# Optimization experiments

Hardware: AMD Instinct MI355X
Metric: run time of the kernel (lower is better)

Reference implementation:

```python
import jax, jax.numpy as jnp
import numpy as np

N_HEADS = 8
TANH_CLIP = 10.0
NEG = -1e9  # finite stand-in for -inf so log_softmax/vjp stay NaN-free


def setup_inputs() -> dict:
    key = jax.random.key(0)
    ks = jax.random.split(key, 8)
    B, N, D = 256, 1000, 128
    embeddings = jax.random.normal(ks[0], (B, N, D), dtype=jnp.float32)
    W_node = jax.random.normal(ks[1], (D, 3 * D), dtype=jnp.float32) * (1.0 / np.sqrt(D))
    W_fixed = jax.random.normal(ks[2], (D, D), dtype=jnp.float32) * (1.0 / np.sqrt(D))
    W_step = jax.random.normal(ks[3], (2 * D, D), dtype=jnp.float32) * (1.0 / np.sqrt(2 * D))
    W_out = jax.random.normal(ks[4], (D, D), dtype=jnp.float32) * (1.0 / np.sqrt(D))
    first_idx = jax.random.randint(ks[5], (B,), 0, N)
    last_idx = jax.random.randint(ks[6], (B,), 0, N)
    mask = jax.random.randint(ks[7], (B, N), 0, 2).astype(jnp.bool_)
    mask = mask.at[:, 0].set(False)  # guarantee at least one feasible node
    return {"embeddings": embeddings, "W_node": W_node, "W_fixed": W_fixed,
            "W_step": W_step, "W_out": W_out, "first_idx": first_idx,
            "last_idx": last_idx, "mask": mask}


def reference(embeddings, W_node, W_fixed, W_step, W_out, first_idx, last_idx, mask):
    # One pointer-network decode step (TSP variant of AttentionModel._get_log_p),
    # including the _precompute projections.
    B, N, D = embeddings.shape
    H = N_HEADS
    dk = D // H

    # _precompute: fixed context + glimpse K/V + logit key
    graph_embed = embeddings.mean(axis=1)                       # [B, D]
    fixed_ctx = graph_embed @ W_fixed                           # [B, D]
    kvl = embeddings @ W_node                                   # [B, N, 3D]
    K, V, logit_K = jnp.split(kvl, 3, axis=-1)                  # each [B, N, D]

    # step context: cat(first-node emb, last-node emb) -> project to D
    b = jnp.arange(B)
    step_ctx = jnp.concatenate([embeddings[b, first_idx], embeddings[b, last_idx]], axis=-1)  # [B, 2D]
    q = fixed_ctx + step_ctx @ W_step                           # [B, D]

    # masked multi-head glimpse attention (q_len = 1)
    qh = q.reshape(B, H, dk)                                    # [B, H, dk]
    Kh = K.reshape(B, N, H, dk)
    Vh = V.reshape(B, N, H, dk)
    compat = jnp.einsum('bhd,bnhd->bhn', qh, Kh) / np.sqrt(dk)  # [B, H, N]
    compat = jnp.where(mask[:, None, :], NEG, compat)           # mask_inner
    attn = jax.nn.softmax(compat, axis=-1)
    heads = jnp.einsum('bhn,bnhd->bhd', attn, Vh)               # [B, H, dk]
    glimpse = heads.reshape(B, D) @ W_out                       # [B, D]

    # single-head logit attention with tanh clipping
    logits = jnp.einsum('bd,bnd->bn', glimpse, logit_K) / np.sqrt(D)  # [B, N]
    logits = jnp.tanh(logits) * TANH_CLIP
    logits = jnp.where(mask, NEG, logits)                       # mask_logits
    return jax.nn.log_softmax(logits, axis=-1)                  # [B, N]
```

## Files before the change

### kernel.cpp

```cpp
#include <hip/hip_runtime.h>


#define NEG (-1e9f)

__global__ __launch_bounds__(1024) void k_fused(
    const float* __restrict__ E, const float* __restrict__ Wn,
    const float* __restrict__ Wf, const float* __restrict__ Ws,
    const float* __restrict__ Wo,
    const int* __restrict__ fi, const int* __restrict__ li,
    const int* __restrict__ maskI, const unsigned char* __restrict__ maskB,
    float* __restrict__ out)
{
    const int b = blockIdx.x;
    const int t = threadIdx.x;

    __shared__ float4 Et[4096];
    __shared__ float4 qk4[256];
    __shared__ float4 pt4[256];
    __shared__ float4 EbarF4[256];
    __shared__ float4 mu4[32], e14[32], e24[32], gp4[32];
    __shared__ float q[128], heads[128], gl[128];
    __shared__ float qred[8][128];
    __shared__ float ct[128 * 9];
    __shared__ float redh[72];
    __shared__ float mh[8], lh[8], al[8];
    __shared__ float red[16];
    __shared__ float stat[2];
    __shared__ int flagS;

    float* const mu = (float*)mu4;
    float* const e1 = (float*)e14;
    float* const e2 = (float*)e24;
    float* const gp = (float*)gp4;
    float* const pt = (float*)pt4;
    float* const EbarF = (float*)EbarF4;
    float* const qkf = (float*)qk4;

    const float4* E4 = (const float4*)(E + (size_t)b * 128000);

    if (t == 0) flagS = 0;
    const uint4 dv = ((const uint4*)maskI)[t];
    const unsigned det = (dv.x | dv.y | dv.z | dv.w) & 0xFFFFFF00u;

    {
        const int cm = t & 31, sm = t >> 5;
        float4 acc = make_float4(0.f, 0.f, 0.f, 0.f);
        for (int r = sm; r < 1000; r += 32) {
            const float4 v = E4[r * 32 + cm];
            acc.x += v.x; acc.y += v.y; acc.z += v.z; acc.w += v.w;
        }
        Et[t] = acc;
    }
    if (t >= 512 && t < 544) {
        e14[t - 512] = E4[fi[b] * 32 + (t - 512)];
    } else if (t >= 544 && t < 576) {
        e24[t - 544] = E4[li[b] * 32 + (t - 544)];
    }
    __syncthreads();
    if (det) atomicOr(&flagS, 1);
    if (t < 32) {
        float4 acc = Et[t];
        #pragma unroll
        for (int s = 1; s < 32; ++s) {
            const float4 v = Et[s * 32 + t];
            acc.x += v.x; acc.y += v.y; acc.z += v.z; acc.w += v.w;
        }
        const float inv = 1.0f / 1000.0f;
        mu4[t] = make_float4(acc.x * inv, acc.y * inv, acc.z * inv, acc.w * inv);
    }
    __syncthreads();

    {
        const int part = t >> 7, d = t & 127;
        float acc = 0.f;
        const int k0 = part * 48;
        for (int k = k0; k < k0 + 48; ++k) {
            const float s = (k < 128) ? mu[k] : (k < 256 ? e1[k - 128] : e2[k - 256]);
            const float w = (k < 128) ? Wf[k * 128 + d] : Ws[(k - 128) * 128 + d];
            acc += s * w;
        }
        qred[part][d] = acc;
    }
    __syncthreads();
    if (t < 128) {
        float acc = 0.f;
        #pragma unroll
        for (int p = 0; p < 8; ++p) acc += qred[p][t];
        q[t] = acc;
    }
    __syncthreads();
    {
        const int j = t & 127, cg = t >> 7;
        const float qj = q[j];
        for (int c0 = 0; c0 < 128; c0 += 8) {
            const int c = c0 + cg;
            float v = Wn[c * 384 + j] * qj;
            v += __shfl_down(v, 8, 16);
            v += __shfl_down(v, 4, 16);
            v += __shfl_down(v, 2, 16);
            v += __shfl_down(v, 1, 16);
            if ((j & 15) == 0) {
                const int h = j >> 4, s = c >> 2;
                qkf[h * 128 + (s ^ (s >> 2)) * 4 + (c & 3)] = v * 0.25f;
            }
        }
    }
    __syncthreads();

    const bool useB = (flagS != 0);

    if (t < 8) { mh[t] = -3e38f; lh[t] = 0.f; }
    float4 eacc[8];
    #pragma unroll
    for (int h = 0; h < 8; ++h) eacc[h] = make_float4(0.f, 0.f, 0.f, 0.f);
    const int c4 = t & 31, sl = t >> 5;
    const int rr = t >> 3, qq = t & 7;

    for (int tile = 0; tile < 8; ++tile) {
        const int r0 = tile * 128;
        {
            const int g = r0 + rr;
            float4 v[4];
            if (g < 1000) {
                #pragma unroll
                for (int i = 0; i < 4; ++i) v[i] = E4[g * 32 + qq * 4 + i];
            } else {
                #pragma unroll
                for (int i = 0; i < 4; ++i) v[i] = make_float4(0.f, 0.f, 0.f, 0.f);
            }
            float pch[8];
            #pragma unroll
            for (int h = 0; h < 8; ++h) pch[h] = 0.f;
            #pragma unroll
            for (int i = 0; i < 4; ++i) {
                const int grp = qq * 4 + i;
                Et[rr * 32 + (grp ^ (rr & 7))] = v[i];
                const int sg = grp ^ (grp >> 2);
                #pragma unroll
                for (int h = 0; h < 8; ++h) {
                    const float4 w = qk4[h * 32 + sg];
                    pch[h] += v[i].x * w.x + v[i].y * w.y + v[i].z * w.z + v[i].w * w.w;
                }
            }
            #pragma unroll
            for (int m = 1; m <= 4; m <<= 1) {
                #pragma unroll
                for (int h = 0; h < 8; ++h) pch[h] += __shfl_xor(pch[h], m, 64);
            }
            bool msk = (g >= 1000);
            if (!msk) msk = useB ? (maskB[b * 1000 + g] != 0)
                                 : (maskI[b * 1000 + g] != 0);
            ct[rr * 9 + qq] = msk ? NEG : pch[qq];
        }
        __syncthreads();
        if (t < 64) {
            const int h = t & 7, part = t >> 3;
            float mt = -3e38f;
            const int rb = part * 16;
            for (int r = 0; r < 16; ++r) mt = fmaxf(mt, ct[(rb + r) * 9 + h]);
            redh[part * 9 + h] = mt;
        }
        __syncthreads();
        if (t < 8) {
            float mt = redh[t];
            for (int p = 1; p < 8; ++p) mt = fmaxf(mt, redh[p * 9 + t]);
            const float mnew = fmaxf(mh[t], mt);
            al[t] = __expf(mh[t] - mnew);
            mh[t] = mnew;
        }
        __syncthreads();
        {
            const int row = t >> 3, h = t & 7;
            pt[row * 8 + h] = __expf(ct[row * 9 + h] - mh[h]);
        }
        __syncthreads();
        {
            #pragma unroll
            for (int h = 0; h < 8; ++h) {
                const float a = al[h];
                eacc[h].x *= a; eacc[h].y *= a; eacc[h].z *= a; eacc[h].w *= a;
            }
            #pragma unroll
            for (int j = 0; j < 4; ++j) {
                const int r = sl * 4 + j;
                const float4 ev = Et[r * 32 + (c4 ^ (r & 7))];
                const float4 p0 = pt4[r * 2];
                const float4 p1 = pt4[r * 2 + 1];
                eacc[0].x += p0.x * ev.x; eacc[0].y += p0.x * ev.y; eacc[0].z += p0.x * ev.z; eacc[0].w += p0.x * ev.w;
                eacc[1].x += p0.y * ev.x; eacc[1].y += p0.y * ev.y; eacc[1].z += p0.y * ev.z; eacc[1].w += p0.y * ev.w;
                eacc[2].x += p0.z * ev.x; eacc[2].y += p0.z * ev.y; eacc[2].z += p0.z * ev.z; eacc[2].w += p0.z * ev.w;
                eacc[3].x += p0.w * ev.x; eacc[3].y += p0.w * ev.y; eacc[3].z += p0.w * ev.z; eacc[3].w += p0.w * ev.w;
                eacc[4].x += p1.x * ev.x; eacc[4].y += p1.x * ev.y; eacc[4].z += p1.x * ev.z; eacc[4].w += p1.x * ev.w;
                eacc[5].x += p1.y * ev.x; eacc[5].y += p1.y * ev.y; eacc[5].z += p1.y * ev.z; eacc[5].w += p1.y * ev.w;
                eacc[6].x += p1.z * ev.x; eacc[6].y += p1.z * ev.y; eacc[6].z += p1.z * ev.z; eacc[6].w += p1.z * ev.w;
                eacc[7].x += p1.w * ev.x; eacc[7].y += p1.w * ev.y; eacc[7].z += p1.w * ev.z; eacc[7].w += p1.w * ev.w;
            }
        }
        if (t < 64) {
            const int h = t & 7, part = t >> 3;
            float s = 0.f;
            const int rb = part * 16;
            for (int r = 0; r < 16; ++r) s += pt[(rb + r) * 8 + h];
            redh[part * 9 + h] = s;
        }
        __syncthreads();
        if (t < 8) {
            float s = 0.f;
            for (int p = 0; p < 8; ++p) s += redh[p * 9 + t];
            lh[t] = lh[t] * al[t] + s;
        }
    }

    if (sl >= 16) {
        #pragma unroll
        for (int h = 0; h < 8; ++h) Et[(sl - 16) * 256 + h * 32 + c4] = eacc[h];
    }
    __syncthreads();
    if (sl < 16) {
        #pragma unroll
        for (int h = 0; h < 8; ++h) {
            const float4 o = Et[sl * 256 + h * 32 + c4];
            eacc[h].x += o.x; eacc[h].y += o.y; eacc[h].z += o.z; eacc[h].w += o.w;
            Et[sl * 256 + h * 32 + c4] = eacc[h];
        }
    }
    __syncthreads();
    if (t < 256) {
        const int h = t >> 5, cc = t & 31;
        float4 s = make_float4(0.f, 0.f, 0.f, 0.f);
        #pragma unroll
        for (int s2 = 0; s2 < 16; ++s2) {
            const float4 v = Et[s2 * 256 + h * 32 + cc];
            s.x += v.x; s.y += v.y; s.z += v.z; s.w += v.w;
        }
        const float invl = 1.0f / lh[h];
        EbarF4[h * 32 + cc] = make_float4(s.x * invl, s.y * invl, s.z * invl, s.w * invl);
    }
    __syncthreads();

    {
        const int part = t >> 7, d = t & 127, h = d >> 4;
        float acc = 0.f;
        const int c0 = part * 16;
        for (int c = c0; c < c0 + 16; ++c) acc += EbarF[h * 128 + c] * Wn[c * 384 + 128 + d];
        qred[part][d] = acc;
    }
    __syncthreads();
    if (t < 128) {
        float acc = 0.f;
        #pragma unroll
        for (int p = 0; p < 8; ++p) acc += qred[p][t];
        heads[t] = acc;
    }
    __syncthreads();
    {
        const int part = t >> 7, d = t & 127;
        float acc = 0.f;
        const int j0 = part * 16;
        for (int j = j0; j < j0 + 16; ++j) acc += heads[j] * Wo[j * 128 + d];
        qred[part][d] = acc;
    }
    __syncthreads();
    if (t < 128) {
        float acc = 0.f;
        #pragma unroll
        for (int p = 0; p < 8; ++p) acc += qred[p][t];
        gl[t] = acc;
    }
    __syncthreads();
    {
        const int part = t >> 7, c = t & 127;
        float acc = 0.f;
        const int d0 = part * 16;
        for (int d = d0; d < d0 + 16; ++d) acc += Wn[c * 384 + 256 + d] * gl[d];
        qred[part][c] = acc;
    }
    __syncthreads();
    if (t < 128) {
        float acc = 0.f;
        #pragma unroll
        for (int p = 0; p < 8; ++p) acc += qred[p][t];
        gp[t] = acc * 0.08838834764831845f;
    }
    __syncthreads();

    {
        const int row = t >> 3, sub = t & 7;
        for (int tile = 0; tile < 8; ++tile) {
            const int g = tile * 128 + row;
            float acc = 0.f;
            if (g < 1000) {
                #pragma unroll
                for (int i = 0; i < 4; ++i) {
                    const float4 v = E4[g * 32 + sub * 4 + i];
                    const float4 w = gp4[sub * 4 + i];
                    acc += v.x * w.x + v.y * w.y + v.z * w.z + v.w * w.w;
                }
            }
            ct[row * 9 + sub] = acc;
            __syncthreads();
            if (t < 128) {
                const int g2 = tile * 128 + t;
                if (g2 < 1000) {
                    float s = 0.f;
                    #pragma unroll
                    for (int k = 0; k < 8; ++k) s += ct[t * 9 + k];
                    float zz = 10.0f * tanhf(s);
                    const bool m = useB ? (maskB[b * 1000 + g2] != 0)
                                        : (maskI[b * 1000 + g2] != 0);
                    if (m) zz = NEG;
                    pt[g2] = zz;
                }
            }
            __syncthreads();
        }
    }
    float v = (t < 1000) ? pt[t] : -3e38f;
    #pragma unroll
    for (int off = 32; off > 0; off >>= 1) v = fmaxf(v, __shfl_down(v, off, 64));
    if ((t & 63) == 0) red[t >> 6] = v;
    __syncthreads();
    if (t == 0) {
        float m = red[0];
        for (int i = 1; i < 16; ++i) m = fmaxf(m, red[i]);
        stat[0] = m;
    }
    __syncthreads();
    float sv = (t < 1000) ? __expf(pt[t] - stat[0]) : 0.f;
    #pragma unroll
    for (int off = 32; off > 0; off >>= 1) sv += __shfl_down(sv, off, 64);
    if ((t & 63) == 0) red[t >> 6] = sv;
    __syncthreads();
    if (t == 0) {
        float s = 0.f;
        for (int i = 0; i < 16; ++i) s += red[i];
        stat[1] = stat[0] + __logf(s);
    }
    __syncthreads();
    if (t < 1000)
        out[(size_t)b * 1000 + t] = pt[t] - stat[1];
}

extern "C" void kernel_launch(void* const* d_in, const int* in_sizes, int n_in,
                              void* d_out, int out_size, void* d_ws, size_t ws_size,
                              hipStream_t stream) {
    const float* E  = (const float*)d_in[0];
    const float* Wn = (const float*)d_in[1];
    const float* Wf = (const float*)d_in[2];
    const float* Ws = (const float*)d_in[3];
    const float* Wo = (const float*)d_in[4];
    const int*   fi = (const int*)d_in[5];
    const int*   li = (const int*)d_in[6];
    const int*   maskI = (const int*)d_in[7];
    const unsigned char* maskB = (const unsigned char*)d_in[7];
    float* out = (float*)d_out;

    k_fused<<<256, 1024, 0, stream>>>(E, Wn, Wf, Ws, Wo, fi, li, maskI, maskB, out);
}
```

Measured before the change: 281.8 us.

## Prefetch next embedding tile, fuse softmax reductions, and drop barriers in decode loop

Register-prefetches the next 128-row embedding tile while the current tile is processed, and loads the first tile before the mean-pooling pass. The per-tile max and sum reductions now use wave shuffles instead of two-stage shared-memory reductions. Exponentials are recomputed inline in the weighted-sum loop rather than staged through shared memory, which removes several barriers per tile. The logit pass also reduces with shuffles and no per-tile barriers. In exchange it raises register pressure at 1024 threads and duplicates the exp work.

```diff
diff --git a/kernel.cpp b/kernel.cpp
--- a/kernel.cpp
+++ b/kernel.cpp
@@ -22,7 +22,6 @@
     __shared__ float q[128], heads[128], gl[128];
     __shared__ float qred[8][128];
     __shared__ float ct[128 * 9];
-    __shared__ float redh[72];
     __shared__ float mh[8], lh[8], al[8];
     __shared__ float red[16];
     __shared__ float stat[2];
@@ -41,6 +40,13 @@
     if (t == 0) flagS = 0;
     const uint4 dv = ((const uint4*)maskI)[t];
     const unsigned det = (dv.x | dv.y | dv.z | dv.w) & 0xFFFFFF00u;
+
+    const int rr = t >> 3, qq = t & 7;
+    const int c4 = t & 31, sl = t >> 5;
+
+    float4 vcur[4];
+    #pragma unroll
+    for (int i = 0; i < 4; ++i) vcur[i] = E4[rr * 32 + qq * 4 + i];
 
     {
         const int cm = t & 31, sm = t >> 5;
@@ -105,41 +111,41 @@
             }
         }
     }
+    if (t < 8) { mh[t] = -3e38f; lh[t] = 0.f; }
     __syncthreads();
 
     const bool useB = (flagS != 0);
 
-    if (t < 8) { mh[t] = -3e38f; lh[t] = 0.f; }
     float4 eacc[8];
     #pragma unroll
     for (int h = 0; h < 8; ++h) eacc[h] = make_float4(0.f, 0.f, 0.f, 0.f);
-    const int c4 = t & 31, sl = t >> 5;
-    const int rr = t >> 3, qq = t & 7;
 
     for (int tile = 0; tile < 8; ++tile) {
-        const int r0 = tile * 128;
+        float4 vnext[4];
+        if (tile < 7) {
+            const int gn = (tile + 1) * 128 + rr;
+            if (gn < 1000) {
+                #pragma unroll
+                for (int i = 0; i < 4; ++i) vnext[i] = E4[gn * 32 + qq * 4 + i];
+            } else {
+                #pragma unroll
+                for (int i = 0; i < 4; ++i) vnext[i] = make_float4(0.f, 0.f, 0.f, 0.f);
+            }
+        }
         {
-            const int g = r0 + rr;
-            float4 v[4];
-            if (g < 1000) {
-                #pragma unroll
-                for (int i = 0; i < 4; ++i) v[i] = E4[g * 32 + qq * 4 + i];
-            } else {
-                #pragma unroll
-                for (int i = 0; i < 4; ++i) v[i] = make_float4(0.f, 0.f, 0.f, 0.f);
-            }
+            const int g = tile * 128 + rr;
             float pch[8];
             #pragma unroll
             for (int h = 0; h < 8; ++h) pch[h] = 0.f;
             #pragma unroll
             for (int i = 0; i < 4; ++i) {
                 const int grp = qq * 4 + i;
-                Et[rr * 32 + (grp ^ (rr & 7))] = v[i];
+                Et[rr * 32 + (grp ^ (rr & 7))] = vcur[i];
                 const int sg = grp ^ (grp >> 2);
                 #pragma unroll
                 for (int h = 0; h < 8; ++h) {
                     const float4 w = qk4[h * 32 + sg];
-                    pch[h] += v[i].x * w.x + v[i].y * w.y + v[i].z * w.z + v[i].w * w.w;
+                    pch[h] += vcur[i].x * w.x + vcur[i].y * w.y + vcur[i].z * w.z + vcur[i].w * w.w;
                 }
             }
             #pragma unroll
@@ -154,61 +160,57 @@
         }
         __syncthreads();
         if (t < 64) {
-            const int h = t & 7, part = t >> 3;
+            const int h = t >> 3, j = t & 7;
             float mt = -3e38f;
-            const int rb = part * 16;
-            for (int r = 0; r < 16; ++r) mt = fmaxf(mt, ct[(rb + r) * 9 + h]);
-            redh[part * 9 + h] = mt;
-        }
-        __syncthreads();
-        if (t < 8) {
-            float mt = redh[t];
-            for (int p = 1; p < 8; ++p) mt = fmaxf(mt, redh[p * 9 + t]);
-            const float mnew = fmaxf(mh[t], mt);
-            al[t] = __expf(mh[t] - mnew);
-            mh[t] = mnew;
+            for (int r = j; r < 128; r += 8) mt = fmaxf(mt, ct[r * 9 + h]);
+            mt = fmaxf(mt, __shfl_xor(mt, 1, 64));
+            mt = fmaxf(mt, __shfl_xor(mt, 2, 64));
+            mt = fmaxf(mt, __shfl_xor(mt, 4, 64));
+            if (j == 0) {
+                const float mnew = fmaxf(mh[h], mt);
+                al[h] = __expf(mh[h] - mnew);
+                mh[h] = mnew;
+            }
         }
         __syncthreads();
         {
-            const int row = t >> 3, h = t & 7;
-            pt[row * 8 + h] = __expf(ct[row * 9 + h] - mh[h]);
+            float alr[8], mhr[8];
+            #pragma unroll
+            for (int h = 0; h < 8; ++h) { alr[h] = al[h]; mhr[h] = mh[h]; }
+            #pragma unroll
+            for (int h = 0; h < 8; ++h) {
+                eacc[h].x *= alr[h]; eacc[h].y *= alr[h];
+                eacc[h].z *= alr[h]; eacc[h].w *= alr[h];
+            }
+            #pragma unroll
+            for (int j2 = 0; j2 < 4; ++j2) {
+                const int r = sl * 4 + j2;
+                const float4 ev = Et[r * 32 + (c4 ^ (r & 7))];
+                float p[8];
+                #pragma unroll
+                for (int h = 0; h < 8; ++h) p[h] = __expf(ct[r * 9 + h] - mhr[h]);
+                #pragma unroll
+                for (int h = 0; h < 8; ++h) {
+                    eacc[h].x += p[h] * ev.x; eacc[h].y += p[h] * ev.y;
+                    eacc[h].z += p[h] * ev.z; eacc[h].w += p[h] * ev.w;
+                }
+            }
+        }
+        if (t < 64) {
+            const int h = t >> 3, j = t & 7;
+            const float mhh = mh[h];
+            float s = 0.f;
+            for (int r = j; r < 128; r += 8) s += __expf(ct[r * 9 + h] - mhh);
+            s += __shfl_xor(s, 1, 64);
+            s += __shfl_xor(s, 2, 64);
+            s += __shfl_xor(s, 4, 64);
+            if (j == 0) lh[h] = lh[h] * al[h] + s;
+        }
+        if (tile < 7) {
+            #pragma unroll
+            for (int i = 0; i < 4; ++i) vcur[i] = vnext[i];
         }
         __syncthreads();
-        {
-            #pragma unroll
-            for (int h = 0; h < 8; ++h) {
-                const float a = al[h];
-                eacc[h].x *= a; eacc[h].y *= a; eacc[h].z *= a; eacc[h].w *= a;
-            }
-            #pragma unroll
-            for (int j = 0; j < 4; ++j) {
-                const int r = sl * 4 + j;
-                const float4 ev = Et[r * 32 + (c4 ^ (r & 7))];
-                const float4 p0 = pt4[r * 2];
-                const float4 p1 = pt4[r * 2 + 1];
-                eacc[0].x += p0.x * ev.x; eacc[0].y += p0.x * ev.y; eacc[0].z += p0.x * ev.z; eacc[0].w += p0.x * ev.w;
-                eacc[1].x += p0.y * ev.x; eacc[1].y += p0.y * ev.y; eacc[1].z += p0.y * ev.z; eacc[1].w += p0.y * ev.w;
-                eacc[2].x += p0.z * ev.x; eacc[2].y += p0.z * ev.y; eacc[2].z += p0.z * ev.z; eacc[2].w += p0.z * ev.w;
-                eacc[3].x += p0.w * ev.x; eacc[3].y += p0.w * ev.y; eacc[3].z += p0.w * ev.z; eacc[3].w += p0.w * ev.w;
-                eacc[4].x += p1.x * ev.x; eacc[4].y += p1.x * ev.y; eacc[4].z += p1.x * ev.z; eacc[4].w += p1.x * ev.w;
-                eacc[5].x += p1.y * ev.x; eacc[5].y += p1.y * ev.y; eacc[5].z += p1.y * ev.z; eacc[5].w += p1.y * ev.w;
-                eacc[6].x += p1.z * ev.x; eacc[6].y += p1.z * ev.y; eacc[6].z += p1.z * ev.z; eacc[6].w += p1.z * ev.w;
-                eacc[7].x += p1.w * ev.x; eacc[7].y += p1.w * ev.y; eacc[7].z += p1.w * ev.z; eacc[7].w += p1.w * ev.w;
-            }
-        }
-        if (t < 64) {
-            const int h = t & 7, part = t >> 3;
-            float s = 0.f;
-            const int rb = part * 16;
-            for (int r = 0; r < 16; ++r) s += pt[(rb + r) * 8 + h];
-            redh[part * 9 + h] = s;
-        }
-        __syncthreads();
-        if (t < 8) {
-            float s = 0.f;
-            for (int p = 0; p < 8; ++p) s += redh[p * 9 + t];
-            lh[t] = lh[t] * al[t] + s;
-        }
     }
 
     if (sl >= 16) {
@@ -284,37 +286,29 @@
     }
     __syncthreads();
 
-    {
-        const int row = t >> 3, sub = t & 7;
-        for (int tile = 0; tile < 8; ++tile) {
-            const int g = tile * 128 + row;
-            float acc = 0.f;
-            if (g < 1000) {
-                #pragma unroll
-                for (int i = 0; i < 4; ++i) {
-                    const float4 v = E4[g * 32 + sub * 4 + i];
-                    const float4 w = gp4[sub * 4 + i];
-                    acc += v.x * w.x + v.y * w.y + v.z * w.z + v.w * w.w;
-                }
-            }
-            ct[row * 9 + sub] = acc;
-            __syncthreads();
-            if (t < 128) {
-                const int g2 = tile * 128 + t;
-                if (g2 < 1000) {
-                    float s = 0.f;
-                    #pragma unroll
-                    for (int k = 0; k < 8; ++k) s += ct[t * 9 + k];
-                    float zz = 10.0f * tanhf(s);
-                    const bool m = useB ? (maskB[b * 1000 + g2] != 0)
-                                        : (maskI[b * 1000 + g2] != 0);
-                    if (m) zz = NEG;
-                    pt[g2] = zz;
-                }
-            }
-            __syncthreads();
-        }
-    }
+    for (int tile = 0; tile < 8; ++tile) {
+        const int g = tile * 128 + rr;
+        float acc = 0.f;
+        if (g < 1000) {
+            #pragma unroll
+            for (int i = 0; i < 4; ++i) {
+                const float4 v = E4[g * 32 + qq * 4 + i];
+                const float4 w = gp4[qq * 4 + i];
+                acc += v.x * w.x + v.y * w.y + v.z * w.z + v.w * w.w;
+            }
+        }
+        acc += __shfl_xor(acc, 1, 64);
+        acc += __shfl_xor(acc, 2, 64);
+        acc += __shfl_xor(acc, 4, 64);
+        if (qq == 0 && g < 1000) {
+            float zz = 10.0f * tanhf(acc);
+            const bool m = useB ? (maskB[b * 1000 + g] != 0)
+                                : (maskI[b * 1000 + g] != 0);
+            if (m) zz = NEG;
+            pt[g] = zz;
+        }
+    }
+    __syncthreads();
     float v = (t < 1000) ? pt[t] : -3e38f;
     #pragma unroll
     for (int off = 32; off > 0; off >>= 1) v = fmaxf(v, __shfl_down(v, off, 64));
```

New measurement: 401.1 us. 1.42x slower.
